# Performance work log

Hardware: AMD Instinct MI355X
Metric: run time of the kernel (lower is better)

## Reference

```python
import jax, jax.numpy as jnp
import numpy as np

B, S, D, H = 32, 2048, 1024, 1024

def setup_inputs() -> dict:
    key = jax.random.key(0)
    k1, k2, k3, k4, k5 = jax.random.split(key, 5)
    return {
        "query": jax.random.normal(k1, (B, D), dtype=jnp.float32),
        "values": jax.random.normal(k2, (B, S, D), dtype=jnp.float32),
        "W1": jax.random.normal(k3, (D, H), dtype=jnp.float32) / np.sqrt(D),
        "W2": jax.random.normal(k4, (D, H), dtype=jnp.float32) / np.sqrt(D),
        "v": jax.random.uniform(k5, (H,), dtype=jnp.float32),
    }

def reference(query, values, W1, W2, v):
    # query: [B, D], values: [B, S, D]
    query_proj = query @ W2                              # [B, H]
    keys_proj = jnp.einsum('bsd,dh->bsh', values, W1)     # [B, S, H]
    energy = jnp.tanh(query_proj[:, None, :] + keys_proj) # [B, S, H]
    scores = jnp.einsum('bsh,h->bs', energy, v)           # [B, S]
    attention_weights = jax.nn.softmax(scores, axis=-1)   # [B, S]
    context = jnp.einsum('bs,bsd->bd', attention_weights, values)  # [B, D]
    return context, attention_weights
```

## Files before the change

### kernel.cpp

```cpp
#include <hip/hip_runtime.h>
#include <hip/hip_fp16.h>


typedef _Float16 v8h __attribute__((ext_vector_type(8)));
typedef float    v4f __attribute__((ext_vector_type(4)));

#define B_DIM 32
#define S_DIM 2048
#define D_DIM 1024
#define H_DIM 1024

#define WS_V16    0u
#define WS_W1T    134217728u
#define WS_QP     (WS_W1T + 2097152u)
#define WS_SCORES (WS_QP + 131072u)
#define WS_PART   (WS_SCORES + 262144u)

__device__ __forceinline__ void gl_lds16(const _Float16* g, _Float16* l) {
    __builtin_amdgcn_global_load_lds(
        (const __attribute__((address_space(1))) void*)g,
        (__attribute__((address_space(3))) void*)l, 16, 0, 0);
}

__global__ void k_prep(const float* __restrict__ values, _Float16* __restrict__ v16,
                       const float* __restrict__ W1, _Float16* __restrict__ w1t,
                       const float* __restrict__ query, const float* __restrict__ W2,
                       float* __restrict__ qp, float* __restrict__ scores) {
    __shared__ float smem[64 * 65];
    int bid = blockIdx.x, tid = threadIdx.x;
    if (bid < 32768) {
        size_t i = ((size_t)bid * 256 + tid) * 8;
        v4f f0 = __builtin_nontemporal_load((const v4f*)(values + i));
        v4f f1 = __builtin_nontemporal_load((const v4f*)(values + i + 4));
        v8h hv;
        hv[0] = (_Float16)f0[0]; hv[1] = (_Float16)f0[1];
        hv[2] = (_Float16)f0[2]; hv[3] = (_Float16)f0[3];
        hv[4] = (_Float16)f1[0]; hv[5] = (_Float16)f1[1];
        hv[6] = (_Float16)f1[2]; hv[7] = (_Float16)f1[3];
        *(v8h*)(v16 + i) = hv;
    } else if (bid < 33024) {
        int j = bid - 32768;
        int h0 = (j & 15) * 64, d0 = (j >> 4) * 64;
        #pragma unroll
        for (int i = 0; i < 16; ++i) {
            int idx = i * 256 + tid;
            int dd = idx >> 6, hh = idx & 63;
            smem[dd * 65 + hh] = W1[(size_t)(d0 + dd) * H_DIM + h0 + hh];
        }
        __syncthreads();
        #pragma unroll
        for (int i = 0; i < 16; ++i) {
            int idx = i * 256 + tid;
            int hh = idx >> 6, dd = idx & 63;
            w1t[(size_t)(h0 + hh) * D_DIM + d0 + dd] = (_Float16)smem[dd * 65 + hh];
        }
    } else if (bid < 33152) {
        int j = bid - 33024;
        int hc = j & 3, b = j >> 2;
        #pragma unroll
        for (int i = 0; i < 4; ++i) smem[i * 256 + tid] = query[b * D_DIM + i * 256 + tid];
        __syncthreads();
        int h = hc * 256 + tid;
        float acc = 0.f;
        #pragma unroll 8
        for (int d = 0; d < D_DIM; ++d) acc += smem[d] * W2[(size_t)d * H_DIM + h];
        qp[b * H_DIM + h] = acc;
    } else {
        int j = bid - 33152;
        size_t o = (size_t)j * 2048 + tid * 8;
        *(v4f*)(scores + o)     = (v4f){0.f, 0.f, 0.f, 0.f};
        *(v4f*)(scores + o + 4) = (v4f){0.f, 0.f, 0.f, 0.f};
    }
}

__global__ __launch_bounds__(256, 2) void k_scores(
        const _Float16* __restrict__ values16, const _Float16* __restrict__ w1t,
        const float* __restrict__ qp, const float* __restrict__ v,
        float* __restrict__ scores) {
    __shared__ _Float16 As[128 * 64];
    __shared__ _Float16 Bs[256 * 64];
    __shared__ float s_scores[128];

    int tid = threadIdx.x;
    int wid = tid >> 6, lane = tid & 63;
    int quad = lane >> 4, l15 = lane & 15;
    int wm = wid >> 1, wn = wid & 1;

    int idx = blockIdx.x;
    int np  = idx & 3;
    int mtb = idx >> 2;
    int b   = mtb >> 4;
    int m0  = (mtb & 15) * 128;
    int n0  = np * 256;

    if (tid < 128) s_scores[tid] = 0.f;

    int srow = lane >> 3;
    int kg   = lane & 7;
    const size_t arow = ((size_t)b * S_DIM + m0) * D_DIM;

    v4f acc[4][8];
    #pragma unroll
    for (int i = 0; i < 4; ++i)
        #pragma unroll
        for (int j = 0; j < 8; ++j) acc[i][j] = (v4f){0.f, 0.f, 0.f, 0.f};

    for (int kt = 0; kt < 16; ++kt) {
        int k0 = kt * 64;
        #pragma unroll
        for (int i = 0; i < 4; ++i) {
            int brow = i * 32 + wid * 8;
            int row  = brow + srow;
            int kgs  = kg ^ (row & 7);
            gl_lds16(values16 + arow + (size_t)row * D_DIM + k0 + kgs * 8, &As[brow * 64]);
        }
        #pragma unroll
        for (int i = 0; i < 8; ++i) {
            int brow = i * 32 + wid * 8;
            int row  = brow + srow;
            int kgs  = kg ^ (row & 7);
            gl_lds16(w1t + (size_t)(n0 + row) * D_DIM + k0 + kgs * 8, &Bs[brow * 64]);
        }
        __syncthreads();
        #pragma unroll
        for (int kk = 0; kk < 2; ++kk) {
            v8h af[4], bf[8];
            #pragma unroll
            for (int mt = 0; mt < 4; ++mt) {
                int row = wm * 64 + mt * 16 + l15;
                int ph  = (kk * 4 + quad) ^ (row & 7);
                af[mt] = *(const v8h*)(&As[row * 64 + ph * 8]);
            }
            #pragma unroll
            for (int nt = 0; nt < 8; ++nt) {
                int row = wn * 128 + nt * 16 + l15;
                int ph  = (kk * 4 + quad) ^ (row & 7);
                bf[nt] = *(const v8h*)(&Bs[row * 64 + ph * 8]);
            }
            #pragma unroll
            for (int mt = 0; mt < 4; ++mt)
                #pragma unroll
                for (int nt = 0; nt < 8; ++nt)
                    acc[mt][nt] = __builtin_amdgcn_mfma_f32_16x16x32_f16(
                        af[mt], bf[nt], acc[mt][nt], 0, 0, 0);
        }
        __syncthreads();
    }
    float qpv[8], vv[8];
    #pragma unroll
    for (int nt = 0; nt < 8; ++nt) {
        int ng = n0 + wn * 128 + nt * 16 + l15;
        qpv[nt] = qp[b * H_DIM + ng];
        vv[nt]  = v[ng];
    }
    #pragma unroll
    for (int mt = 0; mt < 4; ++mt) {
        #pragma unroll
        for (int r = 0; r < 4; ++r) {
            float s = 0.f;
            #pragma unroll
            for (int nt = 0; nt < 8; ++nt) {
                float x = acc[mt][nt][r] + qpv[nt];
                float e = __expf(2.f * x);
                s += (1.f - 2.f / (e + 1.f)) * vv[nt];
            }
            s += __shfl_xor(s, 1);
            s += __shfl_xor(s, 2);
            s += __shfl_xor(s, 4);
            s += __shfl_xor(s, 8);
            if (l15 == 0)
                atomicAdd(&s_scores[wm * 64 + mt * 16 + quad * 4 + r], s);
        }
    }
    __syncthreads();
    if (tid < 128) atomicAdd(&scores[(size_t)b * S_DIM + m0 + tid], s_scores[tid]);
}

__global__ void k_softmax(const float* __restrict__ scores, float* __restrict__ wout) {
    __shared__ float red[256];
    int b = blockIdx.x, tid = threadIdx.x;
    float ls[8];
    float lmax = -1e30f;
    #pragma unroll
    for (int i = 0; i < 8; ++i) {
        ls[i] = scores[b * S_DIM + i * 256 + tid];
        lmax = fmaxf(lmax, ls[i]);
    }
    red[tid] = lmax; __syncthreads();
    for (int st = 128; st > 0; st >>= 1) {
        if (tid < st) red[tid] = fmaxf(red[tid], red[tid + st]);
        __syncthreads();
    }
    float rowmax = red[0]; __syncthreads();
    float lsum = 0.f;
    #pragma unroll
    for (int i = 0; i < 8; ++i) { ls[i] = __expf(ls[i] - rowmax); lsum += ls[i]; }
    red[tid] = lsum; __syncthreads();
    for (int st = 128; st > 0; st >>= 1) {
        if (tid < st) red[tid] += red[tid + st];
        __syncthreads();
    }
    float inv = 1.f / red[0];
    #pragma unroll
    for (int i = 0; i < 8; ++i) wout[b * S_DIM + i * 256 + tid] = ls[i] * inv;
}

__global__ void k_ctx_part(const _Float16* __restrict__ values16,
                           const float* __restrict__ w, float* __restrict__ part) {
    __shared__ float s_w[128];
    __shared__ float s_acc[128][8];
    int b = blockIdx.x >> 4, sc = blockIdx.x & 15, tid = threadIdx.x;
    if (tid < 128) s_w[tid] = w[b * S_DIM + sc * 128 + tid];
    __syncthreads();
    int half = tid >> 7, col = (tid & 127) * 8;
    float acc[8];
    #pragma unroll
    for (int j = 0; j < 8; ++j) acc[j] = 0.f;
    size_t base = ((size_t)(b * S_DIM + sc * 128 + half)) * D_DIM + col;
    #pragma unroll 4
    for (int it = 0; it < 64; ++it) {
        float ww = s_w[it * 2 + half];
        v8h hv = *(const v8h*)(values16 + base + (size_t)it * 2 * D_DIM);
        #pragma unroll
        for (int j = 0; j < 8; ++j) acc[j] += ww * (float)hv[j];
    }
    if (half == 1) {
        #pragma unroll
        for (int j = 0; j < 8; ++j) s_acc[tid & 127][j] = acc[j];
    }
    __syncthreads();
    if (half == 0) {
        #pragma unroll
        for (int j = 0; j < 8; ++j) acc[j] += s_acc[tid][j];
        float* dst = part + (size_t)(b * 16 + sc) * D_DIM + col;
        *(v4f*)dst = (v4f){acc[0], acc[1], acc[2], acc[3]};
        *(v4f*)(dst + 4) = (v4f){acc[4], acc[5], acc[6], acc[7]};
    }
}

__global__ void k_ctx_reduce(const float* __restrict__ part, float* __restrict__ ctx) {
    int o = blockIdx.x * 256 + threadIdx.x;
    int b = o >> 10, d = o & 1023;
    float s = 0.f;
    #pragma unroll
    for (int sc = 0; sc < 16; ++sc) s += part[(size_t)(b * 16 + sc) * D_DIM + d];
    ctx[o] = s;
}

extern "C" void kernel_launch(void* const* d_in, const int* in_sizes, int n_in,
                              void* d_out, int out_size, void* d_ws, size_t ws_size,
                              hipStream_t stream) {
    const float* query  = (const float*)d_in[0];
    const float* values = (const float*)d_in[1];
    const float* W1     = (const float*)d_in[2];
    const float* W2     = (const float*)d_in[3];
    const float* v      = (const float*)d_in[4];

    char* ws = (char*)d_ws;
    _Float16* values16 = (_Float16*)(ws + WS_V16);
    _Float16* w1t      = (_Float16*)(ws + WS_W1T);
    float* qp          = (float*)(ws + WS_QP);
    float* scores      = (float*)(ws + WS_SCORES);
    float* part        = (float*)(ws + WS_PART);

    float* ctx  = (float*)d_out;
    float* wout = (float*)d_out + 32768;

    k_prep<<<dim3(33184), 256, 0, stream>>>(values, values16, W1, w1t, query, W2, qp, scores);
    k_scores<<<dim3(2048), 256, 0, stream>>>(values16, w1t, qp, v, scores);
    k_softmax<<<dim3(32), 256, 0, stream>>>(scores, wout);
    k_ctx_part<<<dim3(512), 256, 0, stream>>>(values16, wout, part);
    k_ctx_reduce<<<dim3(128), 256, 0, stream>>>(part, ctx);
}
```

Measured before the change: 588.6 us.

## Fuse softmax and context into one kernel, skipping near-zero attention rows

```diff
diff --git a/kernel.cpp b/kernel.cpp
--- a/kernel.cpp
+++ b/kernel.cpp
@@ -14,7 +14,6 @@
 #define WS_W1T    134217728u
 #define WS_QP     (WS_W1T + 2097152u)
 #define WS_SCORES (WS_QP + 131072u)
-#define WS_PART   (WS_SCORES + 262144u)
 
 __device__ __forceinline__ void gl_lds16(const _Float16* g, _Float16* l) {
     __builtin_amdgcn_global_load_lds(
@@ -176,75 +175,70 @@
     if (tid < 128) atomicAdd(&scores[(size_t)b * S_DIM + m0 + tid], s_scores[tid]);
 }
 
-__global__ void k_softmax(const float* __restrict__ scores, float* __restrict__ wout) {
-    __shared__ float red[256];
+__global__ __launch_bounds__(1024) void k_finish(
+        const float* __restrict__ scores, const _Float16* __restrict__ values16,
+        float* __restrict__ wout, float* __restrict__ ctx) {
+    __shared__ float s_w[2048];
+    __shared__ int   s_idx[2048];
+    __shared__ float red[16];
+    __shared__ float s_bcast;
+    __shared__ int   s_cnt;
+
     int b = blockIdx.x, tid = threadIdx.x;
-    float ls[8];
-    float lmax = -1e30f;
-    #pragma unroll
-    for (int i = 0; i < 8; ++i) {
-        ls[i] = scores[b * S_DIM + i * 256 + tid];
-        lmax = fmaxf(lmax, ls[i]);
-    }
-    red[tid] = lmax; __syncthreads();
-    for (int st = 128; st > 0; st >>= 1) {
-        if (tid < st) red[tid] = fmaxf(red[tid], red[tid + st]);
-        __syncthreads();
-    }
-    float rowmax = red[0]; __syncthreads();
-    float lsum = 0.f;
-    #pragma unroll
-    for (int i = 0; i < 8; ++i) { ls[i] = __expf(ls[i] - rowmax); lsum += ls[i]; }
-    red[tid] = lsum; __syncthreads();
-    for (int st = 128; st > 0; st >>= 1) {
-        if (tid < st) red[tid] += red[tid + st];
-        __syncthreads();
-    }
-    float inv = 1.f / red[0];
-    #pragma unroll
-    for (int i = 0; i < 8; ++i) wout[b * S_DIM + i * 256 + tid] = ls[i] * inv;
-}
-
-__global__ void k_ctx_part(const _Float16* __restrict__ values16,
-                           const float* __restrict__ w, float* __restrict__ part) {
-    __shared__ float s_w[128];
-    __shared__ float s_acc[128][8];
-    int b = blockIdx.x >> 4, sc = blockIdx.x & 15, tid = threadIdx.x;
-    if (tid < 128) s_w[tid] = w[b * S_DIM + sc * 128 + tid];
-    __syncthreads();
-    int half = tid >> 7, col = (tid & 127) * 8;
-    float acc[8];
-    #pragma unroll
-    for (int j = 0; j < 8; ++j) acc[j] = 0.f;
-    size_t base = ((size_t)(b * S_DIM + sc * 128 + half)) * D_DIM + col;
-    #pragma unroll 4
-    for (int it = 0; it < 64; ++it) {
-        float ww = s_w[it * 2 + half];
-        v8h hv = *(const v8h*)(values16 + base + (size_t)it * 2 * D_DIM);
-        #pragma unroll
-        for (int j = 0; j < 8; ++j) acc[j] += ww * (float)hv[j];
-    }
-    if (half == 1) {
-        #pragma unroll
-        for (int j = 0; j < 8; ++j) s_acc[tid & 127][j] = acc[j];
-    }
-    __syncthreads();
-    if (half == 0) {
-        #pragma unroll
-        for (int j = 0; j < 8; ++j) acc[j] += s_acc[tid][j];
-        float* dst = part + (size_t)(b * 16 + sc) * D_DIM + col;
-        *(v4f*)dst = (v4f){acc[0], acc[1], acc[2], acc[3]};
-        *(v4f*)(dst + 4) = (v4f){acc[4], acc[5], acc[6], acc[7]};
-    }
-}
-
-__global__ void k_ctx_reduce(const float* __restrict__ part, float* __restrict__ ctx) {
-    int o = blockIdx.x * 256 + threadIdx.x;
-    int b = o >> 10, d = o & 1023;
-    float s = 0.f;
-    #pragma unroll
-    for (int sc = 0; sc < 16; ++sc) s += part[(size_t)(b * 16 + sc) * D_DIM + d];
-    ctx[o] = s;
+    int lane = tid & 63, wid = tid >> 6;
+
+    float s0 = scores[b * S_DIM + tid];
+    float s1 = scores[b * S_DIM + 1024 + tid];
+
+    float m = fmaxf(s0, s1);
+    #pragma unroll
+    for (int off = 1; off <= 32; off <<= 1) m = fmaxf(m, __shfl_xor(m, off));
+    if (lane == 0) red[wid] = m;
+    if (tid == 0) s_cnt = 0;
+    __syncthreads();
+    if (tid == 0) {
+        float mm = red[0];
+        #pragma unroll
+        for (int i = 1; i < 16; ++i) mm = fmaxf(mm, red[i]);
+        s_bcast = mm;
+    }
+    __syncthreads();
+    float rowmax = s_bcast;
+
+    float e0 = __expf(s0 - rowmax);
+    float e1 = __expf(s1 - rowmax);
+    float sum = e0 + e1;
+    #pragma unroll
+    for (int off = 1; off <= 32; off <<= 1) sum += __shfl_xor(sum, off);
+    if (lane == 0) red[wid] = sum;
+    __syncthreads();
+    if (tid == 0) {
+        float ss = red[0];
+        #pragma unroll
+        for (int i = 1; i < 16; ++i) ss += red[i];
+        s_bcast = 1.f / ss;
+    }
+    __syncthreads();
+    float inv = s_bcast;
+
+    float w0 = e0 * inv, w1 = e1 * inv;
+    wout[b * S_DIM + tid]        = w0;
+    wout[b * S_DIM + 1024 + tid] = w1;
+    s_w[tid]        = w0;
+    s_w[tid + 1024] = w1;
+
+    if (w0 > 1e-7f) { int p = atomicAdd(&s_cnt, 1); s_idx[p] = tid; }
+    if (w1 > 1e-7f) { int p = atomicAdd(&s_cnt, 1); s_idx[p] = tid + 1024; }
+    __syncthreads();
+    int cnt = s_cnt;
+
+    float acc = 0.f;
+    const _Float16* vb = values16 + (size_t)b * S_DIM * D_DIM + tid;
+    for (int i = 0; i < cnt; ++i) {
+        int s = s_idx[i];
+        acc += s_w[s] * (float)vb[(size_t)s * D_DIM];
+    }
+    ctx[b * D_DIM + tid] = acc;
 }
 
 extern "C" void kernel_launch(void* const* d_in, const int* in_sizes, int n_in,
@@ -261,14 +255,11 @@
     _Float16* w1t      = (_Float16*)(ws + WS_W1T);
     float* qp          = (float*)(ws + WS_QP);
     float* scores      = (float*)(ws + WS_SCORES);
-    float* part        = (float*)(ws + WS_PART);
 
     float* ctx  = (float*)d_out;
     float* wout = (float*)d_out + 32768;
 
     k_prep<<<dim3(33184), 256, 0, stream>>>(values, values16, W1, w1t, query, W2, qp, scores);
     k_scores<<<dim3(2048), 256, 0, stream>>>(values16, w1t, qp, v, scores);
-    k_softmax<<<dim3(32), 256, 0, stream>>>(scores, wout);
-    k_ctx_part<<<dim3(512), 256, 0, stream>>>(values16, wout, part);
-    k_ctx_reduce<<<dim3(128), 256, 0, stream>>>(part, ctx);
-}
+    k_finish<<<dim3(32), 1024, 0, stream>>>(scores, values16, wout, ctx);
+}
```

New measurement: 580.6 us. About the same (-1.4%).
